# Optimization experiments

Measured on AMD Instinct MI355X. Metric: run time of the kernel, lower is better.

The kernel has to match this reference:

```python
import jax, jax.numpy as jnp
import numpy as np

NUM_NODES = 65536      # 16 graphs x 4096 nodes
NODES_PER_GRAPH = 4096
NUM_GRAPHS = 16
NUM_EDGES = 1048576    # avg degree 16
DIM = 64


def setup_inputs() -> dict:
    key = jax.random.key(0)
    ks = jax.random.split(key, 10)
    # edges constrained within each component graph (batched-graph semantics)
    eper = NUM_EDGES // NUM_GRAPHS
    gid = np.repeat(np.arange(NUM_GRAPHS), eper)
    rng = np.random.default_rng(0)
    src = jnp.asarray(rng.integers(0, NODES_PER_GRAPH, NUM_EDGES) + gid * NODES_PER_GRAPH, dtype=jnp.int64)
    dst = jnp.asarray(rng.integers(0, NODES_PER_GRAPH, NUM_EDGES) + gid * NODES_PER_GRAPH, dtype=jnp.int64)
    s = 1.0 / np.sqrt(DIM)
    return {
        "x": jax.random.normal(ks[0], (NUM_NODES, DIM), dtype=jnp.float32),
        "W1": jax.random.normal(ks[1], (DIM, DIM), dtype=jnp.float32) * s,
        "b1": jnp.zeros((DIM,), dtype=jnp.float32),
        "W2": jax.random.normal(ks[2], (DIM, DIM), dtype=jnp.float32) * s,
        "b2": jnp.zeros((DIM,), dtype=jnp.float32),
        "W3": jax.random.normal(ks[3], (DIM, DIM), dtype=jnp.float32) * s,
        "b3": jnp.zeros((DIM,), dtype=jnp.float32),
        "src": src,
        "dst": dst,
        "num_graphs": NUM_GRAPHS,
    }


def _sym_norms(src, dst, n):
    ones = jnp.ones(src.shape[0], dtype=jnp.float32)
    deg_out = jax.ops.segment_sum(ones, src, num_segments=n)
    deg_in = jax.ops.segment_sum(ones, dst, num_segments=n)
    inv_sqrt = lambda d: jnp.where(d > 0, d, 1.0) ** -0.5 * (d > 0)
    return inv_sqrt(deg_out), inv_sqrt(deg_in)


def _graph_conv(x, W, b, src, dst, norm_src, norm_dst, n):
    # DGL GraphConv, norm='both': h = D_in^{-1/2} A D_out^{-1/2} (X W) + b
    h = (x * norm_src[:, None]) @ W          # [N, D]
    msg = h[src]                              # [E, D] gather
    agg = jax.ops.segment_sum(msg, dst, num_segments=n)  # [N, D] scatter-add
    return agg * norm_dst[:, None] + b


def reference(x, W1, b1, W2, b2, W3, b3, src, dst, num_graphs):
    n = x.shape[0]
    norm_src, norm_dst = _sym_norms(src, dst, n)
    h = _graph_conv(x, W1, b1, src, dst, norm_src, norm_dst, n)
    h = _graph_conv(h, W2, b2, src, dst, norm_src, norm_dst, n)
    h = _graph_conv(h, W3, b3, src, dst, norm_src, norm_dst, n)
    # unbatch + pad to max_num_nodes + stack; equal-size graphs -> pure reshape
    return h.reshape(num_graphs, n // num_graphs, h.shape[-1])
```

## Files before the change

kernel.cpp:

```cpp
#include <hip/hip_runtime.h>
#include <hip/hip_fp16.h>

#define DIM 64
#define NG  16
#define CPG 16
#define NPG 4096
#define LSTR 68
#define HISTB (NG*CPG)
#define GGN 32

__global__ __launch_bounds__(256) void kA_hist(
    const int* __restrict__ src, const int* __restrict__ dst,
    int* __restrict__ hsub, int* __restrict__ dsub, int chunk, int npg)
{
    __shared__ int hs[NPG], hd[NPG];
    const int blk = blockIdx.x;
    const int g = blk / CPG;
    const int t = threadIdx.x;
    const int ebase = blk * chunk;
    const int nbase = g * npg;
    for (int i = t; i < npg; i += 256) { hs[i] = 0; hd[i] = 0; }
    __syncthreads();
    for (int e = t; e < chunk; e += 256) {
        atomicAdd(&hs[src[ebase + e] - nbase], 1);
        atomicAdd(&hd[dst[ebase + e] - nbase], 1);
    }
    __syncthreads();
    for (int i = t; i < npg; i += 256) {
        hsub[blk * npg + i] = hs[i];
        dsub[blk * npg + i] = hd[i];
    }
}

__global__ __launch_bounds__(1024) void k2_scan(
    const int* __restrict__ hsub, int* __restrict__ dsub,
    float* __restrict__ ns, float* __restrict__ nd,
    int* __restrict__ rowptr, int epg, int npg, int N, int E)
{
    __shared__ int ddeg[NPG];
    __shared__ int wsum[16];
    const int g = blockIdx.x;
    const int t = threadIdx.x;
    const int nbase = g * npg;
    const int ebase = g * epg;
    for (int i = t; i < npg; i += 1024) {
        int sd = 0, dd = 0;
#pragma unroll
        for (int k = 0; k < CPG; ++k) {
            sd += hsub[(g * CPG + k) * npg + i];
            dd += dsub[(g * CPG + k) * npg + i];
        }
        ns[nbase + i] = sd > 0 ? rsqrtf((float)sd) : 0.0f;
        nd[nbase + i] = dd > 0 ? rsqrtf((float)dd) : 0.0f;
        ddeg[i] = dd;
    }
    __syncthreads();
    const int i0 = 4 * t;
    int d0 = ddeg[i0], d1 = ddeg[i0 + 1], d2 = ddeg[i0 + 2], d3 = ddeg[i0 + 3];
    int s4 = d0 + d1 + d2 + d3;
    const int lane = t & 63, wid = t >> 6;
    int v = s4;
#pragma unroll
    for (int off = 1; off < 64; off <<= 1) {
        int u = __shfl_up(v, off, 64);
        if (lane >= off) v += u;
    }
    if (lane == 63) wsum[wid] = v;
    __syncthreads();
    if (t < 16) {
        int w = wsum[t];
#pragma unroll
        for (int off = 1; off < 16; off <<= 1) {
            int u = __shfl_up(w, off, 16);
            if (t >= off) w += u;
        }
        wsum[t] = w;
    }
    __syncthreads();
    int incl = v + (wid > 0 ? wsum[wid - 1] : 0);
    int c = ebase + incl - s4;
    rowptr[nbase + i0    ] = c; ddeg[i0    ] = c; c += d0;
    rowptr[nbase + i0 + 1] = c; ddeg[i0 + 1] = c; c += d1;
    rowptr[nbase + i0 + 2] = c; ddeg[i0 + 2] = c; c += d2;
    rowptr[nbase + i0 + 3] = c; ddeg[i0 + 3] = c;
    if (g == 0 && t == 0) rowptr[N] = E;
    __syncthreads();
    for (int i = t; i < npg; i += 1024) {
        int cc = ddeg[i];
#pragma unroll
        for (int k = 0; k < CPG; ++k) {
            int* p = &dsub[(g * CPG + k) * npg + i];
            int old = *p; *p = cc; cc += old;
        }
    }
}

__global__ __launch_bounds__(256) void kC_gemm_fill(
    const int* __restrict__ src, const int* __restrict__ dst,
    const int* __restrict__ dsub, int* __restrict__ ssrc, int chunk, int npg,
    const float* __restrict__ x, const float* __restrict__ W1,
    const float* __restrict__ ns, __half* __restrict__ hF, int swiz)
{
    __shared__ float smem[64 * LSTR + 32 * LSTR];
    const int tid = threadIdx.x;
    if ((int)blockIdx.x < HISTB) {
        int* cur = (int*)smem;
        const int blk = blockIdx.x;
        const int g = blk / CPG;
        const int ebase = blk * chunk;
        const int nbase = g * npg;
        for (int i = tid; i < npg; i += 256) cur[i] = dsub[blk * npg + i];
        __syncthreads();
        for (int e = tid; e < chunk; e += 256) {
            int s = src[ebase + e];
            int d = dst[ebase + e] - nbase;
            int pos = atomicAdd(&cur[d], 1);
            ssrc[pos] = s;
        }
    } else {
        float* Wt = smem;
        float* xs = Wt + 64 * LSTR;
        int blk = blockIdx.x - HISTB;
        if (swiz) {
            int xg = blk & 7;
            int j = blk >> 3;
            int g = xg + ((j >> 7) << 3);
            blk = (g << 7) + (j & 127);
        }
        const int row0 = blk * 32;
        for (int i = tid; i < 64 * 64; i += 256) {
            int k = i >> 6, c = i & 63;
            Wt[c * LSTR + k] = W1[i];
        }
        for (int i = tid; i < 32 * 64; i += 256) {
            int r = i >> 6, c = i & 63;
            int row = row0 + r;
            xs[r * LSTR + c] = x[(size_t)row * 64 + c] * ns[row];
        }
        __syncthreads();
        const int c0 = tid & 31;
        const int r0 = tid >> 5;
        float acc[4][2] = {};
#pragma unroll
        for (int k = 0; k < 64; k += 4) {
            float4 w0 = *(const float4*)&Wt[(c0     ) * LSTR + k];
            float4 w1 = *(const float4*)&Wt[(c0 + 32) * LSTR + k];
#pragma unroll
            for (int rr = 0; rr < 4; ++rr) {
                float4 xv = *(const float4*)&xs[(r0 + 8 * rr) * LSTR + k];
                acc[rr][0] += xv.x * w0.x + xv.y * w0.y + xv.z * w0.z + xv.w * w0.w;
                acc[rr][1] += xv.x * w1.x + xv.y * w1.y + xv.z * w1.z + xv.w * w1.w;
            }
        }
#pragma unroll
        for (int rr = 0; rr < 4; ++rr) {
            int row = row0 + r0 + 8 * rr;
            hF[(size_t)row * 64 + c0     ] = __float2half_rn(acc[rr][0]);
            hF[(size_t)row * 64 + c0 + 32] = __float2half_rn(acc[rr][1]);
        }
    }
}

__device__ __forceinline__ void acc_u4(float4& A, float4& B, uint4 u)
{
    __half2 h0 = *(__half2*)&u.x;
    __half2 h1 = *(__half2*)&u.y;
    __half2 h2 = *(__half2*)&u.z;
    __half2 h3 = *(__half2*)&u.w;
    float2 f0 = __half22float2(h0), f1 = __half22float2(h1);
    float2 f2 = __half22float2(h2), f3 = __half22float2(h3);
    A.x += f0.x; A.y += f0.y; A.z += f1.x; A.w += f1.y;
    B.x += f2.x; B.y += f2.y; B.z += f3.x; B.w += f3.y;
}

__device__ __forceinline__ void acc_u4s(float4& A, float4& B, uint4 u, float s)
{
    __half2 h0 = *(__half2*)&u.x;
    __half2 h1 = *(__half2*)&u.y;
    __half2 h2 = *(__half2*)&u.z;
    __half2 h3 = *(__half2*)&u.w;
    float2 f0 = __half22float2(h0), f1 = __half22float2(h1);
    float2 f2 = __half22float2(h2), f3 = __half22float2(h3);
    A.x += s * f0.x; A.y += s * f0.y; A.z += s * f1.x; A.w += s * f1.y;
    B.x += s * f2.x; B.y += s * f2.y; B.z += s * f3.x; B.w += s * f3.y;
}

__device__ __forceinline__ void gather_node(
    const __half* __restrict__ h, const int* __restrict__ ssrc,
    int beg, int end, int sub, float4& A, float4& B)
{
    const size_t off = (size_t)sub * 8;
    int j = beg;
    const int last = end - 8;
    if (j <= last) {
        int s0 = ssrc[j+0], s1 = ssrc[j+1], s2 = ssrc[j+2], s3 = ssrc[j+3];
        int s4 = ssrc[j+4], s5 = ssrc[j+5], s6 = ssrc[j+6], s7 = ssrc[j+7];
        for (;;) {
            uint4 u0 = *(const uint4*)(h + (size_t)s0 * 64 + off);
            uint4 u1 = *(const uint4*)(h + (size_t)s1 * 64 + off);
            uint4 u2 = *(const uint4*)(h + (size_t)s2 * 64 + off);
            uint4 u3 = *(const uint4*)(h + (size_t)s3 * 64 + off);
            uint4 u4 = *(const uint4*)(h + (size_t)s4 * 64 + off);
            uint4 u5 = *(const uint4*)(h + (size_t)s5 * 64 + off);
            uint4 u6 = *(const uint4*)(h + (size_t)s6 * 64 + off);
            uint4 u7 = *(const uint4*)(h + (size_t)s7 * 64 + off);
            j += 8;
            bool more = (j <= last);
            int p = more ? j : beg;
            int n0 = ssrc[p+0], n1 = ssrc[p+1], n2 = ssrc[p+2], n3 = ssrc[p+3];
            int n4 = ssrc[p+4], n5 = ssrc[p+5], n6 = ssrc[p+6], n7 = ssrc[p+7];
            acc_u4(A, B, u0); acc_u4(A, B, u1); acc_u4(A, B, u2); acc_u4(A, B, u3);
            acc_u4(A, B, u4); acc_u4(A, B, u5); acc_u4(A, B, u6); acc_u4(A, B, u7);
            if (!more) break;
            s0 = n0; s1 = n1; s2 = n2; s3 = n3;
            s4 = n4; s5 = n5; s6 = n6; s7 = n7;
        }
    }
    int rem = end - j;
    if (rem > 0) {
#pragma unroll
        for (int q = 0; q < 4; ++q) {
            int jj = j + (q < rem ? q : rem - 1);
            int s = ssrc[jj];
            uint4 u = *(const uint4*)(h + (size_t)s * 64 + off);
            acc_u4s(A, B, u, (q < rem) ? 1.0f : 0.0f);
        }
        if (rem > 4) {
#pragma unroll
            for (int q = 4; q < 8; ++q) {
                int jj = j + (q < rem ? q : rem - 1);
                int s = ssrc[jj];
                uint4 u = *(const uint4*)(h + (size_t)s * 64 + off);
                acc_u4s(A, B, u, (q < rem) ? 1.0f : 0.0f);
            }
        }
    }
}

__global__ __launch_bounds__(256) void gg_kernel(
    const __half* __restrict__ h, const int* __restrict__ ssrc,
    const int* __restrict__ rowptr, const float* __restrict__ ns,
    const float* __restrict__ nd, const float* __restrict__ bprev,
    const float* __restrict__ W, __half* __restrict__ hout,
    int N, int swiz)
{
    __shared__ float us[GGN][64];
    int blk = blockIdx.x;
    if (swiz) {
        int xg = blk & 7;
        int j = blk >> 3;
        int g = xg + ((j >> 7) << 3);
        blk = (g << 7) + (j & 127);
    }
    const int tid = threadIdx.x;
    const int wv = tid >> 6;
    const int lane = tid & 63;
    const int grp = lane >> 3;
    const int sub = lane & 7;

    const int nl = wv * 8 + grp;
    const int w = blk * GGN + nl;
    {
        int beg = rowptr[w], end = rowptr[w + 1];
        float4 A = {0.f,0.f,0.f,0.f}, B = {0.f,0.f,0.f,0.f};
        gather_node(h, ssrc, beg, end, sub, A, B);
        float sw = ns[w];
        float alpha = nd[w] * sw;
        float4 bv0 = *(const float4*)(bprev + sub * 8);
        float4 bv1 = *(const float4*)(bprev + sub * 8 + 4);
        float4 u0, u1;
        u0.x = A.x * alpha + sw * bv0.x;
        u0.y = A.y * alpha + sw * bv0.y;
        u0.z = A.z * alpha + sw * bv0.z;
        u0.w = A.w * alpha + sw * bv0.w;
        u1.x = B.x * alpha + sw * bv1.x;
        u1.y = B.y * alpha + sw * bv1.y;
        u1.z = B.z * alpha + sw * bv1.z;
        u1.w = B.w * alpha + sw * bv1.w;
        *(float4*)&us[nl][sub * 8    ] = u0;
        *(float4*)&us[nl][sub * 8 + 4] = u1;
    }
    __syncthreads();
    const int c = tid & 63;
    const int nb = tid >> 6;
    float y[8] = {0.f,0.f,0.f,0.f,0.f,0.f,0.f,0.f};
#pragma unroll
    for (int k = 0; k < 64; k += 4) {
        float w0 = W[(k    ) * 64 + c];
        float w1 = W[(k + 1) * 64 + c];
        float w2 = W[(k + 2) * 64 + c];
        float w3 = W[(k + 3) * 64 + c];
#pragma unroll
        for (int m = 0; m < 8; ++m) {
            const float4 uv = *(const float4*)&us[nb + 4 * m][k];
            y[m] += uv.x * w0 + uv.y * w1 + uv.z * w2 + uv.w * w3;
        }
    }
#pragma unroll
    for (int m = 0; m < 8; ++m) {
        int wo = blk * GGN + nb + 4 * m;
        hout[(size_t)wo * 64 + c] = __float2half_rn(y[m]);
    }
}

__global__ __launch_bounds__(256) void gather_kernel(
    const __half* __restrict__ h, const int* __restrict__ ssrc,
    const int* __restrict__ rowptr, float* __restrict__ out,
    const float* __restrict__ nd, const float* __restrict__ b,
    int N, int swiz)
{
    int blk = blockIdx.x;
    if (swiz) {
        int x = blk & 7;
        int j = blk >> 3;
        int g = x + ((j >> 7) << 3);
        blk = (g << 7) + (j & 127);
    }
    const int wv = threadIdx.x >> 6;
    const int lane = threadIdx.x & 63;
    const int grp = lane >> 3;
    const int sub = lane & 7;
    int w = blk * 32 + wv * 8 + grp;
    if (w >= N) return;
    int beg = rowptr[w], end = rowptr[w + 1];
    float4 A = {0.f,0.f,0.f,0.f}, B = {0.f,0.f,0.f,0.f};
    gather_node(h, ssrc, beg, end, sub, A, B);
    float n = nd[w];
    const float4 bv0 = *(const float4*)(b + sub * 8);
    const float4 bv1 = *(const float4*)(b + sub * 8 + 4);
    A.x = A.x * n + bv0.x; A.y = A.y * n + bv0.y;
    A.z = A.z * n + bv0.z; A.w = A.w * n + bv0.w;
    B.x = B.x * n + bv1.x; B.y = B.y * n + bv1.y;
    B.z = B.z * n + bv1.z; B.w = B.w * n + bv1.w;
    *(float4*)(out + (size_t)w * 64 + sub * 8    ) = A;
    *(float4*)(out + (size_t)w * 64 + sub * 8 + 4) = B;
}

extern "C" void kernel_launch(void* const* d_in, const int* in_sizes, int n_in,
                              void* d_out, int out_size, void* d_ws, size_t ws_size,
                              hipStream_t stream)
{
    const float* x  = (const float*)d_in[0];
    const float* W1 = (const float*)d_in[1];
    const float* b1 = (const float*)d_in[2];
    const float* W2 = (const float*)d_in[3];
    const float* b2 = (const float*)d_in[4];
    const float* W3 = (const float*)d_in[5];
    const float* b3 = (const float*)d_in[6];
    const int*  src = (const int*)d_in[7];
    const int*  dst = (const int*)d_in[8];

    const int E = in_sizes[7];
    const int N = in_sizes[0] / DIM;
    const int epg = E / NG;
    const int npg = N / NG;
    const int chunk = epg / CPG;

    float*  ns     = (float*)d_ws;
    float*  nd     = ns + N;
    __half* hF     = (__half*)(nd + N);
    __half* h2     = hF + (size_t)N * DIM;
    int*    rowptr = (int*)(h2 + (size_t)N * DIM);
    int*    ssrc   = rowptr + N + 1;
    int*    hsub   = ssrc + E;
    int*    dsub   = hsub + (size_t)HISTB * npg;
    float*  agg    = (float*)d_out;

    const int swiz = (N == 65536 && npg == 4096) ? 1 : 0;

    kA_hist<<<HISTB, 256, 0, stream>>>(src, dst, hsub, dsub, chunk, npg);
    k2_scan<<<NG, 1024, 0, stream>>>(
        hsub, dsub, ns, nd, rowptr, epg, npg, N, E);
    kC_gemm_fill<<<HISTB + N / 32, 256, 0, stream>>>(
        src, dst, dsub, ssrc, chunk, npg, x, W1, ns, hF, swiz);

    gg_kernel<<<N / GGN, 256, 0, stream>>>(
        hF, ssrc, rowptr, ns, nd, b1, W2, h2, N, swiz);
    gg_kernel<<<N / GGN, 256, 0, stream>>>(
        h2, ssrc, rowptr, ns, nd, b2, W3, hF, N, swiz);
    gather_kernel<<<N / 32, 256, 0, stream>>>(
        hF, ssrc, rowptr, agg, nd, b3, N, swiz);
}
```

Measured before the change: 195.0 us.

## Sort nodes by in-degree bucket to balance gather work across wavefronts

The scan kernel now buckets each graph's nodes by in-degree (in steps of 8 edges) and writes a per-graph permutation array. The gather and gather-GEMM kernels process nodes in permuted order and write outputs through the permutation. Nodes in the same wavefront then have similar degrees, which is meant to cut divergent loop iterations in the edge gather. The cost is an extra indirection load, scattered output writes and shared-memory atomics in the scan.

```diff
diff --git a/kernel.cpp b/kernel.cpp
--- a/kernel.cpp
+++ b/kernel.cpp
@@ -35,14 +35,17 @@
 __global__ __launch_bounds__(1024) void k2_scan(
     const int* __restrict__ hsub, int* __restrict__ dsub,
     float* __restrict__ ns, float* __restrict__ nd,
-    int* __restrict__ rowptr, int epg, int npg, int N, int E)
+    int* __restrict__ rowptr, int* __restrict__ perm,
+    int epg, int npg, int N, int E)
 {
     __shared__ int ddeg[NPG];
     __shared__ int wsum[16];
+    __shared__ int bcnt[32];
     const int g = blockIdx.x;
     const int t = threadIdx.x;
     const int nbase = g * npg;
     const int ebase = g * epg;
+    if (t < 32) bcnt[t] = 0;
     for (int i = t; i < npg; i += 1024) {
         int sd = 0, dd = 0;
 #pragma unroll
@@ -84,13 +87,30 @@
     rowptr[nbase + i0 + 2] = c; ddeg[i0 + 2] = c; c += d2;
     rowptr[nbase + i0 + 3] = c; ddeg[i0 + 3] = c;
     if (g == 0 && t == 0) rowptr[N] = E;
-    __syncthreads();
+    int b0 = min((d0 + 7) >> 3, 31);
+    int b1 = min((d1 + 7) >> 3, 31);
+    int b2 = min((d2 + 7) >> 3, 31);
+    int b3 = min((d3 + 7) >> 3, 31);
+    atomicAdd(&bcnt[b0], 1); atomicAdd(&bcnt[b1], 1);
+    atomicAdd(&bcnt[b2], 1); atomicAdd(&bcnt[b3], 1);
+    __syncthreads();
+    if (t == 0) {
+        int s = 0;
+#pragma unroll
+        for (int b = 0; b < 32; ++b) { int cc = bcnt[b]; bcnt[b] = s; s += cc; }
+    }
+    __syncthreads();
+    int p;
+    p = atomicAdd(&bcnt[b0], 1); perm[nbase + p] = nbase + i0;
+    p = atomicAdd(&bcnt[b1], 1); perm[nbase + p] = nbase + i0 + 1;
+    p = atomicAdd(&bcnt[b2], 1); perm[nbase + p] = nbase + i0 + 2;
+    p = atomicAdd(&bcnt[b3], 1); perm[nbase + p] = nbase + i0 + 3;
     for (int i = t; i < npg; i += 1024) {
         int cc = ddeg[i];
 #pragma unroll
         for (int k = 0; k < CPG; ++k) {
-            int* p = &dsub[(g * CPG + k) * npg + i];
-            int old = *p; *p = cc; cc += old;
+            int* pp = &dsub[(g * CPG + k) * npg + i];
+            int old = *pp; *pp = cc; cc += old;
         }
     }
 }
@@ -239,10 +259,10 @@
 
 __global__ __launch_bounds__(256) void gg_kernel(
     const __half* __restrict__ h, const int* __restrict__ ssrc,
-    const int* __restrict__ rowptr, const float* __restrict__ ns,
-    const float* __restrict__ nd, const float* __restrict__ bprev,
-    const float* __restrict__ W, __half* __restrict__ hout,
-    int N, int swiz)
+    const int* __restrict__ rowptr, const int* __restrict__ perm,
+    const float* __restrict__ ns, const float* __restrict__ nd,
+    const float* __restrict__ bprev, const float* __restrict__ W,
+    __half* __restrict__ hout, int N, int swiz)
 {
     __shared__ float us[GGN][64];
     int blk = blockIdx.x;
@@ -259,7 +279,7 @@
     const int sub = lane & 7;
 
     const int nl = wv * 8 + grp;
-    const int w = blk * GGN + nl;
+    const int w = perm[blk * GGN + nl];
     {
         int beg = rowptr[w], end = rowptr[w + 1];
         float4 A = {0.f,0.f,0.f,0.f}, B = {0.f,0.f,0.f,0.f};
@@ -298,16 +318,16 @@
     }
 #pragma unroll
     for (int m = 0; m < 8; ++m) {
-        int wo = blk * GGN + nb + 4 * m;
+        int wo = perm[blk * GGN + nb + 4 * m];
         hout[(size_t)wo * 64 + c] = __float2half_rn(y[m]);
     }
 }
 
 __global__ __launch_bounds__(256) void gather_kernel(
     const __half* __restrict__ h, const int* __restrict__ ssrc,
-    const int* __restrict__ rowptr, float* __restrict__ out,
-    const float* __restrict__ nd, const float* __restrict__ b,
-    int N, int swiz)
+    const int* __restrict__ rowptr, const int* __restrict__ perm,
+    float* __restrict__ out, const float* __restrict__ nd,
+    const float* __restrict__ b, int N, int swiz)
 {
     int blk = blockIdx.x;
     if (swiz) {
@@ -320,8 +340,9 @@
     const int lane = threadIdx.x & 63;
     const int grp = lane >> 3;
     const int sub = lane & 7;
-    int w = blk * 32 + wv * 8 + grp;
-    if (w >= N) return;
+    int slot = blk * 32 + wv * 8 + grp;
+    if (slot >= N) return;
+    int w = perm[slot];
     int beg = rowptr[w], end = rowptr[w + 1];
     float4 A = {0.f,0.f,0.f,0.f}, B = {0.f,0.f,0.f,0.f};
     gather_node(h, ssrc, beg, end, sub, A, B);
@@ -361,7 +382,8 @@
     __half* hF     = (__half*)(nd + N);
     __half* h2     = hF + (size_t)N * DIM;
     int*    rowptr = (int*)(h2 + (size_t)N * DIM);
-    int*    ssrc   = rowptr + N + 1;
+    int*    perm   = rowptr + N + 1;
+    int*    ssrc   = perm + N;
     int*    hsub   = ssrc + E;
     int*    dsub   = hsub + (size_t)HISTB * npg;
     float*  agg    = (float*)d_out;
@@ -370,14 +392,14 @@
 
     kA_hist<<<HISTB, 256, 0, stream>>>(src, dst, hsub, dsub, chunk, npg);
     k2_scan<<<NG, 1024, 0, stream>>>(
-        hsub, dsub, ns, nd, rowptr, epg, npg, N, E);
+        hsub, dsub, ns, nd, rowptr, perm, epg, npg, N, E);
     kC_gemm_fill<<<HISTB + N / 32, 256, 0, stream>>>(
         src, dst, dsub, ssrc, chunk, npg, x, W1, ns, hF, swiz);
 
     gg_kernel<<<N / GGN, 256, 0, stream>>>(
-        hF, ssrc, rowptr, ns, nd, b1, W2, h2, N, swiz);
+        hF, ssrc, rowptr, perm, ns, nd, b1, W2, h2, N, swiz);
     gg_kernel<<<N / GGN, 256, 0, stream>>>(
-        h2, ssrc, rowptr, ns, nd, b2, W3, hF, N, swiz);
+        h2, ssrc, rowptr, perm, ns, nd, b2, W3, hF, N, swiz);
     gather_kernel<<<N / 32, 256, 0, stream>>>(
-        hF, ssrc, rowptr, agg, nd, b3, N, swiz);
-}
+        hF, ssrc, rowptr, perm, agg, nd, b3, N, swiz);
+}
```

Result: slower. 201.9 us (+3.5%).
